# Optimization experiments

Hardware: AMD Instinct MI355X
Metric: run time of the kernel (lower is better)

The kernel has to match this reference:

```python
import jax, jax.numpy as jnp
import numpy as np

R = 4          # args.search_range
D = 2 * R + 1  # window size per axis -> D*D = 81 output channels


def setup_inputs() -> dict:
    key = jax.random.key(0)
    k1, k2 = jax.random.split(key)
    B, C, H, W = 4, 128, 64, 128
    src = jax.random.normal(k1, (B, C, H, W), dtype=jnp.float32)
    tgt = jax.random.normal(k2, (B, C, H, W), dtype=jnp.float32)
    return {"src": src, "tgt": tgt}


def reference(src, tgt):
    # Faithful to the torch code: tgt is zero-padded by R on each spatial side,
    # then for output pixel (i, j) the window indices into the PADDED tensor are
    # I in [i-R, i+R], J in [j-R, j+R]. For i < R the index is negative, which in
    # torch wraps around -> reproduce with modular indexing.
    B, C, H, W = src.shape
    tp = jnp.pad(tgt, ((0, 0), (0, 0), (R, R), (R, R)))  # [B,C,H+2R,W+2R]
    Hp, Wp = H + 2 * R, W + 2 * R
    # col_idx[dj, j] = (j - R + dj) mod Wp
    col_idx = (jnp.arange(W)[None, :] - R + jnp.arange(D)[:, None]) % Wp  # [D,W]
    outs = []
    for di in range(D):  # small fixed loop over 9 row offsets
        row_idx = (jnp.arange(H) - R + di) % Hp        # [H]
        t_rows = tp[:, :, row_idx, :]                  # [B,C,H,Wp]
        t_win = t_rows[:, :, :, col_idx]               # [B,C,H,D,W]
        # channel-dot-product per pixel and per column offset
        outs.append(jnp.einsum('bchdw,bchw->bdhw', t_win, src))
    # channel ordering k = di*D + dj matches the original double loop over (I, J)
    return jnp.concatenate(outs, axis=1)  # [B, D*D, H, W]
```

## Files before the change

### kernel.cpp

```cpp
#include <hip/hip_runtime.h>
#include <stdint.h>

#define NB 4
#define NC 128
#define NH 64
#define NW 128
#define HW (NH * NW)
#define ND 9
#define NOUT (ND * ND)
#define CPW 32

__device__ __forceinline__ float pull_and(int byteidx, float v, int m) {
  return __int_as_float(__builtin_amdgcn_ds_bpermute(byteidx, __float_as_int(v)) & m);
}

__global__ __launch_bounds__(256, 4) void costvol_kernel(const float* __restrict__ src,
                                                         const float* __restrict__ tgt,
                                                         float* __restrict__ out) {
  const int tid  = threadIdx.x;
  const int lane = tid & 63;
  const int wave = tid >> 6;
  const int slice = blockIdx.x >> 5;
  const int di = slice % ND;
  const int b  = slice / ND;
  const int hp = blockIdx.x & 31;
  const int h  = (hp << 1) + (lane >> 5);
  const int w0 = (lane & 31) << 2;
  const int y  = h + di - 8;

  float acc[ND][4];
#pragma unroll
  for (int dj = 0; dj < ND; ++dj)
#pragma unroll
    for (int k = 0; k < 4; ++k) acc[dj][k] = 0.0f;

  const int m0 = (w0 >= 8) ? -1 : 0;
  const int m1 = (w0 >= 4) ? -1 : 0;
  const int i2 = ((lane - 2) & 63) << 2;
  const int i1 = ((lane - 1) & 63) << 2;

  if (y >= 0) {
    const float* spc = src + (size_t)((b * NC + wave * CPW) * NH + h) * NW + w0;
    const float* tpc = tgt + (size_t)((b * NC + wave * CPW) * NH + y) * NW + w0;

#pragma unroll 4
    for (int c = 0; c < CPW; ++c) {
      const float4 sv = *(const float4*)spc;
      const float4 t2 = *(const float4*)tpc;

      float t[12];
      t[0]  = pull_and(i2, t2.x, m0);
      t[1]  = pull_and(i2, t2.y, m0);
      t[2]  = pull_and(i2, t2.z, m0);
      t[3]  = pull_and(i2, t2.w, m0);
      t[4]  = pull_and(i1, t2.x, m1);
      t[5]  = pull_and(i1, t2.y, m1);
      t[6]  = pull_and(i1, t2.z, m1);
      t[7]  = pull_and(i1, t2.w, m1);
      t[8]  = t2.x; t[9] = t2.y; t[10] = t2.z; t[11] = t2.w;

#pragma unroll
      for (int dj = 0; dj < ND; ++dj) {
        acc[dj][0] = fmaf(sv.x, t[dj + 0], acc[dj][0]);
        acc[dj][1] = fmaf(sv.y, t[dj + 1], acc[dj][1]);
        acc[dj][2] = fmaf(sv.z, t[dj + 2], acc[dj][2]);
        acc[dj][3] = fmaf(sv.w, t[dj + 3], acc[dj][3]);
      }

      spc += HW;
      tpc += HW;
    }
  }

  __shared__ float lds[4][ND][64][4];
#pragma unroll
  for (int dj = 0; dj < ND; ++dj) {
    float4 v;
    v.x = acc[dj][0]; v.y = acc[dj][1]; v.z = acc[dj][2]; v.w = acc[dj][3];
    *(float4*)&lds[wave][dj][lane][0] = v;
  }
  __syncthreads();

  for (int s = tid; s < ND * 64; s += 256) {
    const int dj = s >> 6;
    const int l  = s & 63;
    const float4 r0 = *(const float4*)&lds[0][dj][l][0];
    const float4 r1 = *(const float4*)&lds[1][dj][l][0];
    const float4 r2 = *(const float4*)&lds[2][dj][l][0];
    const float4 r3 = *(const float4*)&lds[3][dj][l][0];
    float4 o;
    o.x = (r0.x + r1.x) + (r2.x + r3.x);
    o.y = (r0.y + r1.y) + (r2.y + r3.y);
    o.z = (r0.z + r1.z) + (r2.z + r3.z);
    o.w = (r0.w + r1.w) + (r2.w + r3.w);
    const int hh = (hp << 1) + (l >> 5);
    const int ww = (l & 31) << 2;
    *(float4*)(out + (size_t)(((b * NOUT + di * ND + dj) * NH + hh) * NW + ww)) = o;
  }
}

extern "C" void kernel_launch(void* const* d_in, const int* in_sizes, int n_in,
                              void* d_out, int out_size, void* d_ws, size_t ws_size,
                              hipStream_t stream) {
  const float* src = (const float*)d_in[0];
  const float* tgt = (const float*)d_in[1];
  float* out = (float*)d_out;
  costvol_kernel<<<dim3(NB * ND * 32), dim3(256), 0, stream>>>(src, tgt, out);
}
```

Baseline: 94.87 us.

## Compute three row offsets per block to reuse source loads across di

Each block now handles three consecutive row offsets (di) instead of one, so each src float4 load is reused for three target rows, and the grid shrinks threefold. Out-of-range rows are handled with bitmasks instead of a branch, and the LDS reduction runs three times with extra barriers. Accumulator registers triple (108 floats), so launch bounds drop to 2 blocks per SM-equivalent, trading occupancy and grid size (384 blocks) for fewer redundant src loads.

```diff
diff --git a/kernel.cpp b/kernel.cpp
--- a/kernel.cpp
+++ b/kernel.cpp
@@ -9,93 +9,120 @@
 #define ND 9
 #define NOUT (ND * ND)
 #define CPW 32
+#define DT 3
 
 __device__ __forceinline__ float pull_and(int byteidx, float v, int m) {
   return __int_as_float(__builtin_amdgcn_ds_bpermute(byteidx, __float_as_int(v)) & m);
 }
 
-__global__ __launch_bounds__(256, 4) void costvol_kernel(const float* __restrict__ src,
+__global__ __launch_bounds__(256, 2) void costvol_kernel(const float* __restrict__ src,
                                                          const float* __restrict__ tgt,
                                                          float* __restrict__ out) {
   const int tid  = threadIdx.x;
   const int lane = tid & 63;
   const int wave = tid >> 6;
-  const int slice = blockIdx.x >> 5;
-  const int di = slice % ND;
-  const int b  = slice / ND;
-  const int hp = blockIdx.x & 31;
+
+  const int g  = blockIdx.x;
+  const int hp = g & 31;
+  const int q  = g >> 5;
+  const int b  = q / 3;
+  const int d0 = (q % 3) * DT;
+
   const int h  = (hp << 1) + (lane >> 5);
   const int w0 = (lane & 31) << 2;
-  const int y  = h + di - 8;
+  const int ybase = h + d0 - 8;
 
-  float acc[ND][4];
+  float acc[DT][ND][4];
 #pragma unroll
-  for (int dj = 0; dj < ND; ++dj)
+  for (int dt = 0; dt < DT; ++dt)
 #pragma unroll
-    for (int k = 0; k < 4; ++k) acc[dj][k] = 0.0f;
+    for (int dj = 0; dj < ND; ++dj)
+#pragma unroll
+      for (int k = 0; k < 4; ++k) acc[dt][dj][k] = 0.0f;
 
   const int m0 = (w0 >= 8) ? -1 : 0;
   const int m1 = (w0 >= 4) ? -1 : 0;
   const int i2 = ((lane - 2) & 63) << 2;
   const int i1 = ((lane - 1) & 63) << 2;
 
-  if (y >= 0) {
-    const float* spc = src + (size_t)((b * NC + wave * CPW) * NH + h) * NW + w0;
-    const float* tpc = tgt + (size_t)((b * NC + wave * CPW) * NH + y) * NW + w0;
+  int ma[DT], mb[DT], mc[DT];
+  const float* tp[DT];
+#pragma unroll
+  for (int dt = 0; dt < DT; ++dt) {
+    const int y  = ybase + dt;
+    const int mr = (y >= 0) ? -1 : 0;
+    const int yc = (y >= 0) ? y : 0;
+    ma[dt] = m0 & mr;
+    mb[dt] = m1 & mr;
+    mc[dt] = mr;
+    tp[dt] = tgt + (size_t)((b * NC + wave * CPW) * NH + yc) * NW + w0;
+  }
+  const float* spc = src + (size_t)((b * NC + wave * CPW) * NH + h) * NW + w0;
 
-#pragma unroll 4
-    for (int c = 0; c < CPW; ++c) {
-      const float4 sv = *(const float4*)spc;
-      const float4 t2 = *(const float4*)tpc;
+#pragma unroll 2
+  for (int c = 0; c < CPW; ++c) {
+    const float4 sv = *(const float4*)spc;
+
+#pragma unroll
+    for (int dt = 0; dt < DT; ++dt) {
+      const float4 r = *(const float4*)tp[dt];
 
       float t[12];
-      t[0]  = pull_and(i2, t2.x, m0);
-      t[1]  = pull_and(i2, t2.y, m0);
-      t[2]  = pull_and(i2, t2.z, m0);
-      t[3]  = pull_and(i2, t2.w, m0);
-      t[4]  = pull_and(i1, t2.x, m1);
-      t[5]  = pull_and(i1, t2.y, m1);
-      t[6]  = pull_and(i1, t2.z, m1);
-      t[7]  = pull_and(i1, t2.w, m1);
-      t[8]  = t2.x; t[9] = t2.y; t[10] = t2.z; t[11] = t2.w;
+      t[0]  = pull_and(i2, r.x, ma[dt]);
+      t[1]  = pull_and(i2, r.y, ma[dt]);
+      t[2]  = pull_and(i2, r.z, ma[dt]);
+      t[3]  = pull_and(i2, r.w, ma[dt]);
+      t[4]  = pull_and(i1, r.x, mb[dt]);
+      t[5]  = pull_and(i1, r.y, mb[dt]);
+      t[6]  = pull_and(i1, r.z, mb[dt]);
+      t[7]  = pull_and(i1, r.w, mb[dt]);
+      t[8]  = __int_as_float(__float_as_int(r.x) & mc[dt]);
+      t[9]  = __int_as_float(__float_as_int(r.y) & mc[dt]);
+      t[10] = __int_as_float(__float_as_int(r.z) & mc[dt]);
+      t[11] = __int_as_float(__float_as_int(r.w) & mc[dt]);
 
 #pragma unroll
       for (int dj = 0; dj < ND; ++dj) {
-        acc[dj][0] = fmaf(sv.x, t[dj + 0], acc[dj][0]);
-        acc[dj][1] = fmaf(sv.y, t[dj + 1], acc[dj][1]);
-        acc[dj][2] = fmaf(sv.z, t[dj + 2], acc[dj][2]);
-        acc[dj][3] = fmaf(sv.w, t[dj + 3], acc[dj][3]);
+        acc[dt][dj][0] = fmaf(sv.x, t[dj + 0], acc[dt][dj][0]);
+        acc[dt][dj][1] = fmaf(sv.y, t[dj + 1], acc[dt][dj][1]);
+        acc[dt][dj][2] = fmaf(sv.z, t[dj + 2], acc[dt][dj][2]);
+        acc[dt][dj][3] = fmaf(sv.w, t[dj + 3], acc[dt][dj][3]);
       }
-
-      spc += HW;
-      tpc += HW;
+      tp[dt] += HW;
     }
+    spc += HW;
   }
 
   __shared__ float lds[4][ND][64][4];
 #pragma unroll
-  for (int dj = 0; dj < ND; ++dj) {
-    float4 v;
-    v.x = acc[dj][0]; v.y = acc[dj][1]; v.z = acc[dj][2]; v.w = acc[dj][3];
-    *(float4*)&lds[wave][dj][lane][0] = v;
-  }
-  __syncthreads();
+  for (int dt = 0; dt < DT; ++dt) {
+    if (dt) __syncthreads();
+#pragma unroll
+    for (int dj = 0; dj < ND; ++dj) {
+      float4 v;
+      v.x = acc[dt][dj][0]; v.y = acc[dt][dj][1];
+      v.z = acc[dt][dj][2]; v.w = acc[dt][dj][3];
+      *(float4*)&lds[wave][dj][lane][0] = v;
+    }
+    __syncthreads();
 
-  for (int s = tid; s < ND * 64; s += 256) {
-    const int dj = s >> 6;
-    const int l  = s & 63;
-    const float4 r0 = *(const float4*)&lds[0][dj][l][0];
-    const float4 r1 = *(const float4*)&lds[1][dj][l][0];
-    const float4 r2 = *(const float4*)&lds[2][dj][l][0];
-    const float4 r3 = *(const float4*)&lds[3][dj][l][0];
-    float4 o;
-    o.x = (r0.x + r1.x) + (r2.x + r3.x);
-    o.y = (r0.y + r1.y) + (r2.y + r3.y);
-    o.z = (r0.z + r1.z) + (r2.z + r3.z);
-    o.w = (r0.w + r1.w) + (r2.w + r3.w);
-    const int hh = (hp << 1) + (l >> 5);
-    const int ww = (l & 31) << 2;
-    *(float4*)(out + (size_t)(((b * NOUT + di * ND + dj) * NH + hh) * NW + ww)) = o;
+    const int di = d0 + dt;
+    for (int s = tid; s < ND * 64; s += 256) {
+      const int dj = s >> 6;
+      const int l  = s & 63;
+      const float4 r0 = *(const float4*)&lds[0][dj][l][0];
+      const float4 r1 = *(const float4*)&lds[1][dj][l][0];
+      const float4 r2 = *(const float4*)&lds[2][dj][l][0];
+      const float4 r3 = *(const float4*)&lds[3][dj][l][0];
+      float4 o;
+      o.x = (r0.x + r1.x) + (r2.x + r3.x);
+      o.y = (r0.y + r1.y) + (r2.y + r3.y);
+      o.z = (r0.z + r1.z) + (r2.z + r3.z);
+      o.w = (r0.w + r1.w) + (r2.w + r3.w);
+      const int hh = (hp << 1) + (l >> 5);
+      const int ww = (l & 31) << 2;
+      *(float4*)(out + (size_t)(((b * NOUT + di * ND + dj) * NH + hh) * NW + ww)) = o;
+    }
   }
 }
 
@@ -105,5 +132,5 @@
   const float* src = (const float*)d_in[0];
   const float* tgt = (const float*)d_in[1];
   float* out = (float*)d_out;
-  costvol_kernel<<<dim3(NB * ND * 32), dim3(256), 0, stream>>>(src, tgt, out);
+  costvol_kernel<<<dim3(NB * DT * 32), dim3(256), 0, stream>>>(src, tgt, out);
 }
```

New measurement: 115.7 us. 1.22x slower.
